# Optimization experiments

Hardware: AMD Instinct MI355X
Metric: run time of the kernel (lower is better)

The kernel has to match this reference:

```python
import jax, jax.numpy as jnp
import numpy as np

B, C, H, W, L, R = 1, 32, 96, 128, 2, 3
N = 2 * R + 1
EPS = 1e-5


def conv2d(x, w, stride=1, pad=1):
    return jax.lax.conv_general_dilated(
        x, w, (stride, stride), ((pad, pad), (pad, pad)),
        dimension_numbers=('NCHW', 'OIHW', 'NCHW'))


def conv_transpose2d(x, w, stride=2, pad=1):
    # torch ConvTranspose2d semantics; w: [Cin, Cout, kH, kW]
    kh, kw = w.shape[2], w.shape[3]
    wf = jnp.flip(w, (2, 3)).transpose(1, 0, 2, 3)  # [Cout, Cin, kh, kw]
    return jax.lax.conv_general_dilated(
        x, wf, (1, 1),
        ((kh - 1 - pad, kh - 1 - pad), (kw - 1 - pad, kw - 1 - pad)),
        lhs_dilation=(stride, stride),
        dimension_numbers=('NCHW', 'OIHW', 'NCHW'))


def bnorm(x, s, b, m, v):
    # inference-mode BatchNorm2d (fixed running stats)
    inv = s * jax.lax.rsqrt(v + EPS)
    return x * inv[None, :, None, None] + (b - m * inv)[None, :, None, None]


def grid_sample(img, grid):
    # bilinear, align_corners=True, padding_mode='zeros'
    # img [B,C,H,W], grid [B,Hg,Wg,2] (x,y) in [-1,1]
    Bi, Ci, Hi, Wi = img.shape
    gx = (grid[..., 0] + 1.0) * 0.5 * (Wi - 1)
    gy = (grid[..., 1] + 1.0) * 0.5 * (Hi - 1)
    x0 = jnp.floor(gx)
    y0 = jnp.floor(gy)
    wx = (gx - x0)[:, None]  # [B,1,Hg,Wg]
    wy = (gy - y0)[:, None]

    def tap(yf, xf):
        valid = (xf >= 0) & (xf <= Wi - 1) & (yf >= 0) & (yf <= Hi - 1)
        xc = jnp.clip(xf, 0, Wi - 1).astype(jnp.int32)
        yc = jnp.clip(yf, 0, Hi - 1).astype(jnp.int32)
        v = jax.vmap(lambda im, y, x: im[:, y, x])(img, yc, xc)  # [B,C,Hg,Wg]
        return v * valid[:, None].astype(img.dtype)

    v00 = tap(y0, x0)
    v01 = tap(y0, x0 + 1)
    v10 = tap(y0 + 1, x0)
    v11 = tap(y0 + 1, x0 + 1)
    return (v00 * (1 - wx) * (1 - wy) + v01 * wx * (1 - wy)
            + v10 * (1 - wx) * wy + v11 * wx * wy)


def _forward(fmap1_0, fmap1_1, fmap2_0, fmap2_1, coords,
             cw1, cw2, cw3, cw4, ctw5, cw6, cb6,
             bn1s, bn1b, bn1m, bn1v, bn2s, bn2b, bn2m, bn2v,
             bn3s, bn3b, bn3m, bn3v, bn4s, bn4b, bn4m, bn4v,
             bn5s, bn5b, bn5m, bn5v, dap_w):
    n = N
    dx = jnp.linspace(-R, R, n)
    delta = jnp.stack(jnp.meshgrid(dx, dx, indexing='ij'), axis=-1)  # [n,n,2]
    b, _, h, w = coords.shape
    cp = coords.transpose(0, 2, 3, 1)  # [b,h,w,2] (x,y)
    bns = ((bn1s, bn1b, bn1m, bn1v), (bn2s, bn2b, bn2m, bn2v),
           (bn3s, bn3b, bn3m, bn3v), (bn4s, bn4b, bn4m, bn4v),
           (bn5s, bn5b, bn5m, bn5v))
    out = []
    for i, (f1, f2) in enumerate(((fmap1_0, fmap2_0), (fmap1_1, fmap2_1))):
        c, h2, w2 = f1.shape[1], f1.shape[2], f1.shape[3]
        # [b,n,h,n,w,2]: first n axis pairs with h, second with w (as in torch view)
        cent = cp[:, None, :, None, :, :] / (2.0 ** i) + delta[None, :, None, :, None, :]
        gx = 2.0 * cent[..., 0] / (w2 - 1) - 1.0
        gy = 2.0 * cent[..., 1] / (h2 - 1) - 1.0
        grid = jnp.stack([gx, gy], -1).reshape(b, n * h, n * w, 2)
        f2s = grid_sample(f2, grid).reshape(b, c, n, h, n, w)
        f2s = f2s.transpose(0, 2, 4, 1, 3, 5)  # [b,du,dv,c,h,w]
        f1e = jnp.broadcast_to(f1[:, None, None], (b, n, n, c, h, w))
        x = jnp.concatenate([f1e, f2s], axis=3).reshape(b * n * n, 2 * c, h, w)
        # MatchingNet (DICL): conv-bn-relu stack, stride-2 down + transposed up
        x = jax.nn.relu(bnorm(conv2d(x, cw1[i]), *(p[i] for p in bns[0])))
        x = jax.nn.relu(bnorm(conv2d(x, cw2[i], stride=2), *(p[i] for p in bns[1])))
        x = jax.nn.relu(bnorm(conv2d(x, cw3[i]), *(p[i] for p in bns[2])))
        x = jax.nn.relu(bnorm(conv2d(x, cw4[i]), *(p[i] for p in bns[3])))
        x = jax.nn.relu(bnorm(conv_transpose2d(x, ctw5[i]), *(p[i] for p in bns[4])))
        x = conv2d(x, cw6[i]) + cb6[i][None, :, None, None]  # [b*n*n,1,h,w]
        cost = x.reshape(b, n * n, h, w)
        # DisplacementAwareProjection: 1x1 conv over the 49 displacement channels
        cost = jnp.einsum('pq,bqhw->bphw', dap_w[i], cost)
        out.append(cost)
    return jnp.concatenate(out, axis=1)  # [b, L*(2r+1)^2, h, w]


def setup_inputs():
    key = jax.random.key(0)
    ks = jax.random.split(key, 40)

    def rn(k, shape, scale=1.0):
        return jax.random.normal(k, shape, jnp.float32) * scale

    inp = {}
    inp['fmap1_0'] = rn(ks[0], (B, C, H, W))
    inp['fmap2_0'] = rn(ks[1], (B, C, H, W))
    inp['fmap1_1'] = rn(ks[2], (B, C, H, W))
    inp['fmap2_1'] = rn(ks[3], (B, C, H, W))
    gy, gx = jnp.meshgrid(jnp.arange(H, dtype=jnp.float32),
                          jnp.arange(W, dtype=jnp.float32), indexing='ij')
    base = jnp.stack([gx, gy], 0)[None]  # [1,2,H,W] (x,y) pixel coords
    inp['coords'] = base + rn(ks[4], (B, 2, H, W), 2.0)

    def cw(k, co, ci, kk):
        return rn(k, (L, co, ci, kk, kk), 1.0 / np.sqrt(ci * kk * kk))

    inp['cw1'] = cw(ks[5], 96, 2 * C, 3)
    inp['cw2'] = cw(ks[6], 128, 96, 3)
    inp['cw3'] = cw(ks[7], 128, 128, 3)
    inp['cw4'] = cw(ks[8], 64, 128, 3)
    inp['ctw5'] = rn(ks[9], (L, 64, 32, 4, 4), 1.0 / np.sqrt(64 * 16))
    inp['cw6'] = cw(ks[10], 1, 32, 3)
    inp['cb6'] = rn(ks[11], (L, 1), 0.1)
    for j, ch in enumerate((96, 128, 128, 64, 32), start=1):
        k4 = jax.random.split(ks[11 + j], 4)
        inp['bn%ds' % j] = 1.0 + rn(k4[0], (L, ch), 0.1)
        inp['bn%db' % j] = rn(k4[1], (L, ch), 0.1)
        inp['bn%dm' % j] = rn(k4[2], (L, ch), 0.1)
        inp['bn%dv' % j] = 1.0 + rn(k4[3], (L, ch), 0.1) ** 2
    # DAP identity init
    inp['dap_w'] = jnp.tile(jnp.eye(N * N, dtype=jnp.float32)[None], (L, 1, 1))
    return inp


def reference(fmap1_0, fmap1_1, fmap2_0, fmap2_1, coords,
              cw1, cw2, cw3, cw4, ctw5, cw6, cb6,
              bn1s, bn1b, bn1m, bn1v, bn2s, bn2b, bn2m, bn2v,
              bn3s, bn3b, bn3m, bn3v, bn4s, bn4b, bn4m, bn4v,
              bn5s, bn5b, bn5m, bn5v, dap_w):
    return _forward(fmap1_0, fmap1_1, fmap2_0, fmap2_1, coords,
                    cw1, cw2, cw3, cw4, ctw5, cw6, cb6,
                    bn1s, bn1b, bn1m, bn1v, bn2s, bn2b, bn2m, bn2v,
                    bn3s, bn3b, bn3m, bn3v, bn4s, bn4b, bn4m, bn4v,
                    bn5s, bn5b, bn5m, bn5v, dap_w)
```

## Files before the change

### kernel.cpp

```cpp
#include <hip/hip_runtime.h>

#define EPSF 1e-5f

typedef __attribute__((ext_vector_type(8))) short short8;
typedef __attribute__((ext_vector_type(4))) float f32x4;

__device__ __forceinline__ ushort f2bf(float x) {
    union { float f; unsigned u; } c; c.f = x;
    unsigned r = c.u + 0x7FFF + ((c.u >> 16) & 1);
    return (ushort)(r >> 16);
}
__device__ __forceinline__ float bf2f(ushort b) {
    union { unsigned u; float f; } c; c.u = ((unsigned)b) << 16;
    return c.f;
}
__device__ __forceinline__ int swz(int a) {
    return a ^ (((a >> 7) & 7) << 4);
}


__global__ __launch_bounds__(256) void k_repack_conv(
    const float* __restrict__ src, ushort* __restrict__ dst, int CO, int CI)
{
    int idx = blockIdx.x * 256 + threadIdx.x;
    if (idx >= CO * CI * 9) return;
    int co = idx / (CI * 9);
    int rem = idx % (CI * 9);
    int ci = rem / 9, tap = rem % 9;
    dst[((size_t)tap * CO + co) * CI + ci] = f2bf(src[idx]);
}

__global__ __launch_bounds__(256) void k_repack_ct(
    const float* __restrict__ src, ushort* __restrict__ dst)
{
    int idx = blockIdx.x * 256 + threadIdx.x;
    if (idx >= 4 * 4 * 32 * 64) return;
    int ci = idx & 63;
    int t = idx >> 6;
    int co = t & 31; t >>= 5;
    int tap = t & 3;
    int parity = t >> 2;
    int ph = parity >> 1, pw = parity & 1;
    int a = tap >> 1, b = tap & 1;
    int kh = ((ph + 1) & 1) + 2 * a;
    int kw = ((pw + 1) & 1) + 2 * b;
    dst[idx] = f2bf(src[((ci * 32 + co) * 4 + kh) * 4 + kw]);
}

__global__ __launch_bounds__(256) void k_sample_nhwc(
    const float* __restrict__ f1_0, const float* __restrict__ f1_1,
    const float* __restrict__ f2_0, const float* __restrict__ f2_1,
    const float* __restrict__ coords, ushort* __restrict__ x0, int d0)
{
    const int HW = 12288;
    const int sp = blockIdx.x * 256 + threadIdx.x;
    const int slot = blockIdx.z;
    const int p = d0 + slot;
    const int l = p / 49;
    const int d = p - l * 49;
    const int du = d / 7, dv = d % 7;
    const float inv_scale = l ? 0.5f : 1.0f;
    const float* f1 = l ? f1_1 : f1_0;
    const float* f2 = l ? f2_1 : f2_0;

    float cx = coords[sp] * inv_scale + (float)(du - 3);
    float cy = coords[HW + sp] * inv_scale + (float)(dv - 3);
    float xf = floorf(cx), yf = floorf(cy);
    float wx = cx - xf, wy = cy - yf;
    int xi = (int)xf, yi = (int)yf;
    float vx0 = (xf >= 0.f && xf <= 127.f) ? 1.f : 0.f;
    float vx1 = (xf + 1.f >= 0.f && xf + 1.f <= 127.f) ? 1.f : 0.f;
    float vy0 = (yf >= 0.f && yf <= 95.f) ? 1.f : 0.f;
    float vy1 = (yf + 1.f >= 0.f && yf + 1.f <= 95.f) ? 1.f : 0.f;
    int x0i = min(max(xi, 0), 127), x1i = min(max(xi + 1, 0), 127);
    int y0i = min(max(yi, 0), 95),  y1i = min(max(yi + 1, 0), 95);
    float w00 = (1.f - wx) * (1.f - wy) * vx0 * vy0;
    float w01 = wx * (1.f - wy) * vx1 * vy0;
    float w10 = (1.f - wx) * wy * vx0 * vy1;
    float w11 = wx * wy * vx1 * vy1;
    int o00 = y0i * 128 + x0i, o01 = y0i * 128 + x1i;
    int o10 = y1i * 128 + x0i, o11 = y1i * 128 + x1i;

    ushort* dst = x0 + ((size_t)slot * HW + sp) * 64;
    #pragma unroll
    for (int g = 0; g < 4; ++g) {
        uint4 pk;
        uint* pw_ = (uint*)&pk;
        #pragma unroll
        for (int q = 0; q < 4; ++q) {
            int c = g * 8 + q * 2;
            pw_[q] = (uint)f2bf(f1[(size_t)c * HW + sp])
                   | ((uint)f2bf(f1[(size_t)(c + 1) * HW + sp]) << 16);
        }
        *(uint4*)(dst + g * 8) = pk;
    }
    #pragma unroll
    for (int g = 0; g < 4; ++g) {
        uint4 pk;
        uint* pw_ = (uint*)&pk;
        #pragma unroll
        for (int q = 0; q < 4; ++q) {
            uint wv = 0;
            #pragma unroll
            for (int h = 0; h < 2; ++h) {
                int c = g * 8 + q * 2 + h;
                const float* fc = f2 + (size_t)c * HW;
                float s = w00 * fc[o00] + w01 * fc[o01] + w10 * fc[o10] + w11 * fc[o11];
                wv |= ((uint)f2bf(s)) << (16 * h);
            }
            pw_[q] = wv;
        }
        *(uint4*)(dst + 32 + g * 8) = pk;
    }
}

template <int CIN, int COUT, int ROWS, int IH, int IW>
__global__ __launch_bounds__(512) void k_conv_lds8(
    const ushort* __restrict__ in, ushort* __restrict__ out,
    const ushort* __restrict__ wbase, int wlstride,
    const float* __restrict__ bs0, const float* __restrict__ bb0,
    const float* __restrict__ bm0, const float* __restrict__ bv0, int d0)
{
    constexpr int NFT = ROWS / 16;
    constexpr int CC = CIN / 64;
    constexpr int NCT = IW / 64;
    constexpr int AB = 10 * 66 * 128;
    constexpr int PB = 3 * ROWS * 128;
    constexpr int SA = (AB + 8191) / 8192;
    constexpr int SB = (PB + 8191) / 8192;
    constexpr int NPH = 3 * CC;
    __shared__ __align__(16) char smem[AB + 2 * PB];
    char* As = smem;

    const int tid = threadIdx.x;
    const int lane = tid & 63, wid = tid >> 6;
    const int lr = lane & 15, kg = lane >> 4;
    const int rt = (int)blockIdx.x / NCT, ct = (int)blockIdx.x % NCT;
    const int r0 = rt * 8, c0 = ct * 64;
    const int co0 = blockIdx.y * ROWS;
    const int slot = blockIdx.z;
    const int l = (d0 + slot) / 49;

    int aoff[SA]; unsigned awr = 0, avalid = 0;
    #pragma unroll
    for (int i = 0; i < SA; ++i) {
        int lin = i * 8192 + tid * 16;
        bool wr = lin < AB;
        int linc = wr ? lin : 0;
        int pos = linc >> 7;
        int prow = (pos * 994) >> 16;
        int pcol = pos - prow * 66;
        int grow = r0 - 1 + prow, gcol = c0 - 1 + pcol;
        bool ok = wr && ((unsigned)grow < (unsigned)IH) && ((unsigned)gcol < (unsigned)IW);
        if (wr) awr |= 1u << i;
        if (ok) avalid |= 1u << i;
        int growc = min(max(grow, 0), IH - 1), gcolc = min(max(gcol, 0), IW - 1);
        aoff[i] = (growc * IW + gcolc) * CIN + ((linc & 127) >> 1);
    }
    int boff[SB]; unsigned bmask = 0;
    #pragma unroll
    for (int i = 0; i < SB; ++i) {
        int lin = i * 8192 + tid * 16;
        if (lin < PB) bmask |= 1u << i;
        int lc = min(lin, PB - 16);
        int rowidx = lc >> 7;
        int tpg = rowidx / ROWS, r = rowidx - tpg * ROWS;
        boff[i] = (tpg * COUT + co0 + r) * CIN + ((lc & 127) >> 1);
    }

    const ushort* ib = in + (size_t)slot * IH * IW * CIN;
    const ushort* wl = wbase + (size_t)l * wlstride;
    const short8 z8 = {0, 0, 0, 0, 0, 0, 0, 0};

    short8 stgA[SA], stgB[SB];
    auto loadA = [&](int cc) {
        #pragma unroll
        for (int i = 0; i < SA; ++i) {
            if ((avalid >> i) & 1) stgA[i] = *(const short8*)(ib + aoff[i] + cc * 64);
            else stgA[i] = z8;
        }
    };
    auto writeA = [&]() {
        #pragma unroll
        for (int i = 0; i < SA; ++i) {
            int lin = i * 8192 + tid * 16;
            if ((awr >> i) & 1)
                *(short8*)(As + swz(lin)) = stgA[i];
        }
    };
    auto loadB = [&](int ps) {
        int pg = ps % 3, cc = ps / 3;
        const ushort* src = wl + pg * (3 * COUT * CIN) + cc * 64;
        #pragma unroll
        for (int i = 0; i < SB; ++i)
            if ((bmask >> i) & 1) stgB[i] = *(const short8*)(src + boff[i]);
    };
    auto writeB = [&](int ps) {
        char* Bs = smem + AB + (ps & 1) * PB;
        #pragma unroll
        for (int i = 0; i < SB; ++i) {
            int lin = i * 8192 + tid * 16;
            if ((bmask >> i) & 1)
                *(short8*)(Bs + swz(lin)) = stgB[i];
        }
    };

    f32x4 acc[4][NFT];
    #pragma unroll
    for (int mf = 0; mf < 4; ++mf)
        #pragma unroll
        for (int nf = 0; nf < NFT; ++nf)
            acc[mf][nf] = (f32x4){0.f, 0.f, 0.f, 0.f};

    loadA(0); loadB(0);
    writeA(); writeB(0);
    __syncthreads();

    #pragma unroll 1
    for (int ps = 0; ps < NPH; ++ps) {
        const int pg = ps % 3;
        const bool hasNext = (ps + 1 < NPH);
        const bool newA = (CC > 1) && (pg == 2) && hasNext;
        if (hasNext) loadB(ps + 1);
        if (newA) loadA(ps / 3 + 1);

        const char* Bs = smem + AB + (ps & 1) * PB;
        #pragma unroll
        for (int kw = 0; kw < 3; ++kw) {
            const int spb = (wid + pg) * 66 + lr + kw;
            #pragma unroll
            for (int ks = 0; ks < 2; ++ks) {
                short8 a[4];
                #pragma unroll
                for (int mf = 0; mf < 4; ++mf) {
                    int sp = spb + mf * 16;
                    a[mf] = *(const short8*)(As + swz(sp * 128 + ks * 64 + kg * 16));
                }
                #pragma unroll
                for (int nf = 0; nf < NFT; ++nf) {
                    int rb = kw * ROWS + nf * 16 + lr;
                    short8 b = *(const short8*)(Bs + swz(rb * 128 + ks * 64 + kg * 16));
                    #pragma unroll
                    for (int mf = 0; mf < 4; ++mf)
                        acc[mf][nf] = __builtin_amdgcn_mfma_f32_16x16x32_bf16(
                            a[mf], b, acc[mf][nf], 0, 0, 0);
                }
            }
        }

        __syncthreads();
        if (hasNext) writeB(ps + 1);
        if (newA) writeA();
        if (hasNext) __syncthreads();
    }

    const float* bs = bs0 + l * COUT;
    const float* bb = bb0 + l * COUT;
    const float* bm = bm0 + l * COUT;
    const float* bv = bv0 + l * COUT;
    ushort* ob = out + (size_t)slot * IH * IW * COUT;
    const int orow = r0 + wid;
    #pragma unroll
    for (int nf = 0; nf < NFT; ++nf) {
        const int col = co0 + nf * 16 + lr;
        const float inv = bs[col] * rsqrtf(bv[col] + EPSF);
        const float beta = bb[col] - bm[col] * inv;
        #pragma unroll
        for (int mf = 0; mf < 4; ++mf) {
            #pragma unroll
            for (int j = 0; j < 4; ++j) {
                int ocol = c0 + mf * 16 + kg * 4 + j;
                float y = fmaxf(fmaf(acc[mf][nf][j], inv, beta), 0.f);
                ob[((size_t)orow * IW + ocol) * COUT + col] = f2bf(y);
            }
        }
    }
}

__global__ __launch_bounds__(512) void k_conv_s2_8(
    const ushort* __restrict__ in, ushort* __restrict__ out,
    const ushort* __restrict__ wbase, int wlstride,
    const float* __restrict__ bs0, const float* __restrict__ bb0,
    const float* __restrict__ bm0, const float* __restrict__ bv0, int d0)
{
    constexpr int AB = 9 * 130 * 64;
    constexpr int PB = 3 * 128 * 64;
    constexpr int SA = (AB + 8191) / 8192;
    constexpr int SB = PB / 8192;
    constexpr int NPH = 9;
    __shared__ __align__(16) char smem[AB + 2 * PB];
    char* As = smem;

    const int tid = threadIdx.x;
    const int lane = tid & 63, wid = tid >> 6;
    const int lr = lane & 15, kg = lane >> 4;
    const int mw = wid >> 1, ch = wid & 1;
    const int r0 = (int)blockIdx.x * 4;
    const int slot = blockIdx.z;
    const int l = (d0 + slot) / 49;

    int aoff[SA]; unsigned awr = 0, avalid = 0;
    #pragma unroll
    for (int i = 0; i < SA; ++i) {
        int lin = i * 8192 + tid * 16;
        bool wr = lin < AB;
        int linc = wr ? lin : 0;
        int pos = linc >> 6;
        int prow = (pos * 2017) >> 18;
        int pcol = pos - prow * 130;
        int grow = 2 * r0 - 1 + prow, gcol = pcol - 1;
        bool ok = wr && ((unsigned)grow < 96u) && ((unsigned)gcol < 128u);
        if (wr) awr |= 1u << i;
        if (ok) avalid |= 1u << i;
        int growc = min(max(grow, 0), 95), gcolc = min(max(gcol, 0), 127);
        aoff[i] = (growc * 128 + gcolc) * 96 + ((linc & 63) >> 1);
    }
    int boff[SB];
    #pragma unroll
    for (int i = 0; i < SB; ++i) {
        int lin = i * 8192 + tid * 16;
        int rowidx = lin >> 6;
        int tpg = rowidx >> 7, r = rowidx & 127;
        boff[i] = ((tpg * 128 + r) * 96) + ((lin & 63) >> 1);
    }

    const ushort* ib = in + (size_t)slot * 12288 * 96;
    const ushort* wl = wbase + (size_t)l * wlstride;
    const short8 z8 = {0, 0, 0, 0, 0, 0, 0, 0};

    short8 stgA[SA], stgB[SB];
    auto loadA = [&](int cc) {
        #pragma unroll
        for (int i = 0; i < SA; ++i) {
            if ((avalid >> i) & 1) stgA[i] = *(const short8*)(ib + aoff[i] + cc * 32);
            else stgA[i] = z8;
        }
    };
    auto writeA = [&]() {
        #pragma unroll
        for (int i = 0; i < SA; ++i) {
            int lin = i * 8192 + tid * 16;
            if ((awr >> i) & 1)
                *(short8*)(As + swz(lin)) = stgA[i];
        }
    };
    auto loadB = [&](int ps) {
        int pg = ps % 3, cc = ps / 3;
        const ushort* src = wl + pg * (3 * 128 * 96) + cc * 32;
        #pragma unroll
        for (int i = 0; i < SB; ++i)
            stgB[i] = *(const short8*)(src + boff[i]);
    };
    auto writeB = [&](int ps) {
        char* Bs = smem + AB + (ps & 1) * PB;
        #pragma unroll
        for (int i = 0; i < SB; ++i) {
            int lin = i * 8192 + tid * 16;
            *(short8*)(Bs + swz(lin)) = stgB[i];
        }
    };

    f32x4 acc[4][4];
    #pragma unroll
    for (int mf = 0; mf < 4; ++mf)
        #pragma unroll
        for (int nf = 0; nf < 4; ++nf)
            acc[mf][nf] = (f32x4){0.f, 0.f, 0.f, 0.f};

    loadA(0); loadB(0);
    writeA(); writeB(0);
    __syncthreads();

    #pragma unroll 1
    for (int ps = 0; ps < NPH; ++ps) {
        const int pg = ps % 3;
        const bool hasNext = (ps + 1 < NPH);
        const bool newA = (pg == 2) && hasNext;
        if (hasNext) loadB(ps + 1);
        if (newA) loadA(ps / 3 + 1);

        const char* Bs = smem + AB + (ps & 1) * PB;
        #pragma unroll
        for (int kw = 0; kw < 3; ++kw) {
            short8 a[4];
            #pragma unroll
            for (int mf = 0; mf < 4; ++mf) {
                int pos = (2 * mw + pg) * 130 + 2 * (mf * 16 + lr) + kw;
                a[mf] = *(const short8*)(As + swz(pos * 64 + kg * 16));
            }
            #pragma unroll
            for (int nf = 0; nf < 4; ++nf) {
                int rb = kw * 128 + ch * 64 + nf * 16 + lr;
                short8 b = *(const short8*)(Bs + swz(rb * 64 + kg * 16));
                #pragma unroll
                for (int mf = 0; mf < 4; ++mf)
                    acc[mf][nf] = __builtin_amdgcn_mfma_f32_16x16x32_bf16(
                        a[mf], b, acc[mf][nf], 0, 0, 0);
            }
        }

        __syncthreads();
        if (hasNext) writeB(ps + 1);
        if (newA) writeA();
        if (hasNext) __syncthreads();
    }

    const float* bs = bs0 + l * 128;
    const float* bb = bb0 + l * 128;
    const float* bm = bm0 + l * 128;
    const float* bv = bv0 + l * 128;
    ushort* ob = out + (size_t)slot * 3072 * 128;
    const int orow = r0 + mw;
    #pragma unroll
    for (int nf = 0; nf < 4; ++nf) {
        const int col = ch * 64 + nf * 16 + lr;
        const float inv = bs[col] * rsqrtf(bv[col] + EPSF);
        const float beta = bb[col] - bm[col] * inv;
        #pragma unroll
        for (int mf = 0; mf < 4; ++mf) {
            #pragma unroll
            for (int j = 0; j < 4; ++j) {
                int ocol = mf * 16 + kg * 4 + j;
                float y = fmaxf(fmaf(acc[mf][nf][j], inv, beta), 0.f);
                ob[((size_t)orow * 64 + ocol) * 128 + col] = f2bf(y);
            }
        }
    }
}

__global__ __launch_bounds__(256) void k_convt_mfma(
    const ushort* __restrict__ in, ushort* __restrict__ out,
    const ushort* __restrict__ wbase,
    const float* __restrict__ bs0, const float* __restrict__ bb0,
    const float* __restrict__ bm0, const float* __restrict__ bv0, int d0)
{
    constexpr int SLICE = 4 * 32 * 128;
    constexpr int S = 4;
    __shared__ __align__(16) char smem[SLICE];

    const int tid = threadIdx.x;
    const int lane = tid & 63, wid = tid >> 6;
    const int lr = lane & 15, kg = lane >> 4;
    const int m0 = blockIdx.x * 256 + wid * 64;
    const int parity = blockIdx.y;
    const int slot = blockIdx.z;
    const int l = (d0 + slot) / 49;
    const int ph = parity >> 1, pw = parity & 1;
    const int kh0 = (ph + 1) & 1, kw0 = (pw + 1) & 1;

    {
        const char* wsrc = (const char*)(wbase + (size_t)l * (16 * 32 * 64));
        #pragma unroll
        for (int i = 0; i < S; ++i) {
            int lin = i * 4096 + tid * 16;
            int rowidx = lin >> 7;
            int tap = rowidx >> 5, r = rowidx & 31;
            short8 v = *(const short8*)(wsrc
                + (((size_t)(parity * 4 + tap) * 32 + r) * 64) * 2 + (lin & 127));
            *(short8*)(smem + swz(lin)) = v;
        }
    }
    __syncthreads();

    int ihA[4], iwA[4];
    #pragma unroll
    for (int mf = 0; mf < 4; ++mf) {
        int m = m0 + mf * 16 + lr;
        int q = m >> 6, r = m & 63;
        ihA[mf] = (2 * q + ph + 1 - kh0) >> 1;
        iwA[mf] = (2 * r + pw + 1 - kw0) >> 1;
    }
    const ushort* ib = in + (size_t)slot * 3072 * 64;

    const short8 z8 = {0, 0, 0, 0, 0, 0, 0, 0};
    f32x4 acc[4][2];
    #pragma unroll
    for (int mf = 0; mf < 4; ++mf)
        #pragma unroll
        for (int nf = 0; nf < 2; ++nf)
            acc[mf][nf] = (f32x4){0.f, 0.f, 0.f, 0.f};

    #pragma unroll
    for (int a = 0; a < 2; ++a) {
        #pragma unroll
        for (int b2 = 0; b2 < 2; ++b2) {
            int srcoff[4]; bool val[4];
            #pragma unroll
            for (int mf = 0; mf < 4; ++mf) {
                int ih = ihA[mf] - a;
                int iw = iwA[mf] - b2;
                val[mf] = ((unsigned)ih < 48u) && ((unsigned)iw < 64u);
                int ihc = min(max(ih, 0), 47), iwc = min(max(iw, 0), 63);
                srcoff[mf] = (ihc * 64 + iwc) * 64;
            }
            const int tap = a * 2 + b2;
            #pragma unroll
            for (int cc = 0; cc < 2; ++cc) {
                const int kbase = cc * 32 + kg * 8;
                short8 av[4];
                #pragma unroll
                for (int mf = 0; mf < 4; ++mf) {
                    short8 v = *(const short8*)(ib + srcoff[mf] + kbase);
                    av[mf] = val[mf] ? v : z8;
                }
                #pragma unroll
                for (int nf = 0; nf < 2; ++nf) {
                    short8 bfr = *(const short8*)(smem
                        + swz((tap * 32 + nf * 16 + lr) * 128 + cc * 64 + kg * 16));
                    #pragma unroll
                    for (int mf = 0; mf < 4; ++mf)
                        acc[mf][nf] = __builtin_amdgcn_mfma_f32_16x16x32_bf16(
                            av[mf], bfr, acc[mf][nf], 0, 0, 0);
                }
            }
        }
    }

    const float* bs = bs0 + l * 32;
    const float* bb = bb0 + l * 32;
    const float* bm = bm0 + l * 32;
    const float* bv = bv0 + l * 32;
    ushort* ob = out + (size_t)slot * 12288 * 32;
    #pragma unroll
    for (int nf = 0; nf < 2; ++nf) {
        const int col = nf * 16 + lr;
        const float inv = bs[col] * rsqrtf(bv[col] + EPSF);
        const float beta = bb[col] - bm[col] * inv;
        #pragma unroll
        for (int mf = 0; mf < 4; ++mf) {
            #pragma unroll
            for (int j = 0; j < 4; ++j) {
                int m = m0 + mf * 16 + kg * 4 + j;
                int q = m >> 6, r = m & 63;
                int sp = (2 * q + ph) * 128 + (2 * r + pw);
                float y = fmaxf(fmaf(acc[mf][nf][j], inv, beta), 0.f);
                ob[(size_t)sp * 32 + col] = f2bf(y);
            }
        }
    }
}

__global__ __launch_bounds__(256) void k_conv6(
    const ushort* __restrict__ x5, float* __restrict__ cost,
    const float* __restrict__ w0, const float* __restrict__ cb6, int d0)
{
    const int sp = blockIdx.x * 256 + threadIdx.x;
    const int slot = blockIdx.z;
    const int p = d0 + slot;
    const int l = p / 49;
    const float* w = w0 + l * 288;
    const int oh = sp >> 7, ow = sp & 127;
    float acc = 0.f;
    #pragma unroll
    for (int kh = 0; kh < 3; ++kh) {
        const int ih = oh - 1 + kh;
        if (ih < 0 || ih >= 96) continue;
        #pragma unroll
        for (int kw = 0; kw < 3; ++kw) {
            const int iw = ow - 1 + kw;
            if (iw < 0 || iw >= 128) continue;
            const ushort* q = x5 + ((size_t)slot * 12288 + ih * 128 + iw) * 32;
            const int tap = kh * 3 + kw;
            #pragma unroll
            for (int g = 0; g < 4; ++g) {
                uint4 v = *(const uint4*)(q + g * 8);
                const uint* vw = (const uint*)&v;
                #pragma unroll
                for (int t = 0; t < 4; ++t) {
                    int ci = g * 8 + t * 2;
                    acc = fmaf(bf2f((ushort)(vw[t] & 0xFFFF)), w[ci * 9 + tap], acc);
                    acc = fmaf(bf2f((ushort)(vw[t] >> 16)), w[(ci + 1) * 9 + tap], acc);
                }
            }
        }
    }
    cost[(size_t)p * 12288 + sp] = acc + cb6[l];
}

__global__ __launch_bounds__(256) void k_dap(
    const float* __restrict__ cost, const float* __restrict__ dw,
    float* __restrict__ out)
{
    const int sp = blockIdx.x * 256 + threadIdx.x;
    const int p = blockIdx.y;
    const float* dr = dw + p * 49;
    float acc = 0.f;
    #pragma unroll
    for (int q = 0; q < 49; ++q)
        acc = fmaf(dr[q], cost[(size_t)q * 12288 + sp], acc);
    out[(size_t)p * 12288 + sp] = acc;
}

extern "C" void kernel_launch(void* const* d_in, const int* in_sizes, int n_in,
                              void* d_out, int out_size, void* d_ws, size_t ws_size,
                              hipStream_t stream)
{
    const float* fm1_0 = (const float*)d_in[0];
    const float* fm2_0 = (const float*)d_in[1];
    const float* fm1_1 = (const float*)d_in[2];
    const float* fm2_1 = (const float*)d_in[3];
    const float* coords = (const float*)d_in[4];
    const float* cw1  = (const float*)d_in[5];
    const float* cw2  = (const float*)d_in[6];
    const float* cw3  = (const float*)d_in[7];
    const float* cw4  = (const float*)d_in[8];
    const float* ctw5 = (const float*)d_in[9];
    const float* cw6  = (const float*)d_in[10];
    const float* cb6  = (const float*)d_in[11];
    const float* bn[5][4];
    for (int j = 0; j < 5; ++j)
        for (int k = 0; k < 4; ++k)
            bn[j][k] = (const float*)d_in[12 + j * 4 + k];
    const float* dap = (const float*)d_in[32];
    float* out = (float*)d_out;

    const size_t A_US = 786432;
    const size_t B_US = 1179648;
    const size_t W1 = 9 * 96 * 64, W2 = 9 * 128 * 96, W3 = 9 * 128 * 128;
    const size_t W4 = 9 * 64 * 128, W5 = 16 * 32 * 64;
    const size_t W_US = 2 * (W1 + W2 + W3 + W4 + W5);
    const size_t COSTF = (size_t)98 * 12288;

    int DC = 1;
    for (int cand : {98, 66, 49, 42, 33, 25, 17, 13, 9, 7, 5, 3, 2, 1}) {
        size_t need = (A_US + B_US) * (size_t)cand * 2 + W_US * 2 + COSTF * 4 + 4096;
        if (need <= ws_size) { DC = cand; break; }
    }

    ushort* bufA = (ushort*)d_ws;
    ushort* bufB = bufA + A_US * DC;
    ushort* wp = bufB + B_US * DC;
    ushort* wr1 = wp; wp += 2 * W1;
    ushort* wr2 = wp; wp += 2 * W2;
    ushort* wr3 = wp; wp += 2 * W3;
    ushort* wr4 = wp; wp += 2 * W4;
    ushort* wr5 = wp; wp += 2 * W5;
    float* cost = (float*)wp;

    for (int l = 0; l < 2; ++l) {
        k_repack_conv<<<dim3(216), 256, 0, stream>>>(cw1 + (size_t)l * W1, wr1 + l * W1, 96, 64);
        k_repack_conv<<<dim3(432), 256, 0, stream>>>(cw2 + (size_t)l * W2, wr2 + l * W2, 128, 96);
        k_repack_conv<<<dim3(576), 256, 0, stream>>>(cw3 + (size_t)l * W3, wr3 + l * W3, 128, 128);
        k_repack_conv<<<dim3(288), 256, 0, stream>>>(cw4 + (size_t)l * W4, wr4 + l * W4, 64, 128);
        k_repack_ct<<<dim3(128), 256, 0, stream>>>(ctw5 + (size_t)l * W5, wr5 + l * W5);
    }

    for (int d0 = 0; d0 < 98; d0 += DC) {
        const int ndd = min(DC, 98 - d0);
        k_sample_nhwc<<<dim3(48, 1, ndd), 256, 0, stream>>>(
            fm1_0, fm1_1, fm2_0, fm2_1, coords, bufA, d0);
        k_conv_lds8<64, 96, 96, 96, 128>
            <<<dim3(24, 1, ndd), 512, 0, stream>>>(bufA, bufB, wr1, (int)W1,
                bn[0][0], bn[0][1], bn[0][2], bn[0][3], d0);
        k_conv_s2_8<<<dim3(12, 1, ndd), 512, 0, stream>>>(bufB, bufA, wr2, (int)W2,
                bn[1][0], bn[1][1], bn[1][2], bn[1][3], d0);
        k_conv_lds8<128, 128, 64, 48, 64>
            <<<dim3(6, 2, ndd), 512, 0, stream>>>(bufA, bufB, wr3, (int)W3,
                bn[2][0], bn[2][1], bn[2][2], bn[2][3], d0);
        k_conv_lds8<128, 64, 64, 48, 64>
            <<<dim3(6, 1, ndd), 512, 0, stream>>>(bufB, bufA, wr4, (int)W4,
                bn[3][0], bn[3][1], bn[3][2], bn[3][3], d0);
        k_convt_mfma<<<dim3(12, 4, ndd), 256, 0, stream>>>(bufA, bufB, wr5,
                bn[4][0], bn[4][1], bn[4][2], bn[4][3], d0);
        k_conv6<<<dim3(48, 1, ndd), 256, 0, stream>>>(
            bufB, cost, cw6, cb6, d0);
    }
    for (int l = 0; l < 2; ++l)
        k_dap<<<dim3(48, 49), 256, 0, stream>>>(
            cost + (size_t)l * 49 * 12288, dap + (size_t)l * 49 * 49,
            out + (size_t)l * 49 * 12288);
}
```

Baseline: 826.8 us.

## Precompute displacement-invariant fmap1 half of first conv once per level

The first conv's input concatenates fmap1 (identical for all 49 displacements) with sampled fmap2. The fmap1 half's partial conv result is now computed once per level into an fp32 buffer, and each displacement only convolves the 32 sampled channels, starting from that precomputed partial sum. This roughly halves the first conv's MACs and the sampler's writes. In exchange, each block must read a large fp32 accumulator preload, and a new specialized conv kernel with its own epilogue is introduced.

```diff
diff --git a/kernel.cpp b/kernel.cpp
--- a/kernel.cpp
+++ b/kernel.cpp
@@ -47,10 +47,28 @@
     dst[idx] = f2bf(src[((ci * 32 + co) * 4 + kh) * 4 + kw]);
 }
 
+__global__ __launch_bounds__(256) void k_pack_f1(
+    const float* __restrict__ f1, ushort* __restrict__ xf1)
+{
+    const int sp = blockIdx.x * 256 + threadIdx.x;
+    ushort* dst = xf1 + (size_t)sp * 32;
+    #pragma unroll
+    for (int g = 0; g < 4; ++g) {
+        uint4 pk;
+        uint* pw_ = (uint*)&pk;
+        #pragma unroll
+        for (int q = 0; q < 4; ++q) {
+            int c = g * 8 + q * 2;
+            pw_[q] = (uint)f2bf(f1[(size_t)c * 12288 + sp])
+                   | ((uint)f2bf(f1[(size_t)(c + 1) * 12288 + sp]) << 16);
+        }
+        *(uint4*)(dst + g * 8) = pk;
+    }
+}
+
 __global__ __launch_bounds__(256) void k_sample_nhwc(
-    const float* __restrict__ f1_0, const float* __restrict__ f1_1,
     const float* __restrict__ f2_0, const float* __restrict__ f2_1,
-    const float* __restrict__ coords, ushort* __restrict__ x0, int d0)
+    const float* __restrict__ coords, ushort* __restrict__ x0s, int d0)
 {
     const int HW = 12288;
     const int sp = blockIdx.x * 256 + threadIdx.x;
@@ -60,7 +78,6 @@
     const int d = p - l * 49;
     const int du = d / 7, dv = d % 7;
     const float inv_scale = l ? 0.5f : 1.0f;
-    const float* f1 = l ? f1_1 : f1_0;
     const float* f2 = l ? f2_1 : f2_0;
 
     float cx = coords[sp] * inv_scale + (float)(du - 3);
@@ -81,19 +98,7 @@
     int o00 = y0i * 128 + x0i, o01 = y0i * 128 + x1i;
     int o10 = y1i * 128 + x0i, o11 = y1i * 128 + x1i;
 
-    ushort* dst = x0 + ((size_t)slot * HW + sp) * 64;
-    #pragma unroll
-    for (int g = 0; g < 4; ++g) {
-        uint4 pk;
-        uint* pw_ = (uint*)&pk;
-        #pragma unroll
-        for (int q = 0; q < 4; ++q) {
-            int c = g * 8 + q * 2;
-            pw_[q] = (uint)f2bf(f1[(size_t)c * HW + sp])
-                   | ((uint)f2bf(f1[(size_t)(c + 1) * HW + sp]) << 16);
-        }
-        *(uint4*)(dst + g * 8) = pk;
-    }
+    ushort* dst = x0s + ((size_t)slot * HW + sp) * 32;
     #pragma unroll
     for (int g = 0; g < 4; ++g) {
         uint4 pk;
@@ -110,7 +115,154 @@
             }
             pw_[q] = wv;
         }
-        *(uint4*)(dst + 32 + g * 8) = pk;
+        *(uint4*)(dst + g * 8) = pk;
+    }
+}
+
+template <int EPI>
+__global__ __launch_bounds__(512) void k_conv1(
+    const ushort* __restrict__ in,
+    ushort* __restrict__ out,
+    const ushort* __restrict__ wbase,
+    const float* __restrict__ p1,
+    const float* __restrict__ bs0, const float* __restrict__ bb0,
+    const float* __restrict__ bm0, const float* __restrict__ bv0,
+    int d0, int koff)
+{
+    constexpr int AB = 10 * 130 * 64;
+    constexpr int PB = 3 * 96 * 64;
+    __shared__ __align__(16) char smem[AB + 2 * PB];
+    char* As = smem;
+
+    const int tid = threadIdx.x;
+    const int lane = tid & 63, wid = tid >> 6;
+    const int lr = lane & 15, kg = lane >> 4;
+    const int rt = blockIdx.x;
+    const int r0 = rt * 8;
+    const int slot = blockIdx.z;
+    const int l = (d0 + slot) / 49;
+
+    const ushort* ib = in + (size_t)slot * 12288 * 32;
+    const ushort* wl = wbase + (size_t)l * (9 * 96 * 64);
+    const short8 z8 = {0, 0, 0, 0, 0, 0, 0, 0};
+
+    #pragma unroll
+    for (int i = 0; i < 11; ++i) {
+        int lin = i * 8192 + tid * 16;
+        if (lin < AB) {
+            int pos = lin >> 6;
+            int prow = (pos * 2017) >> 18;
+            int pcol = pos - prow * 130;
+            int grow = r0 - 1 + prow, gcol = pcol - 1;
+            bool ok = ((unsigned)grow < 96u) && ((unsigned)gcol < 128u);
+            short8 v = z8;
+            if (ok) v = *(const short8*)(ib + (grow * 128 + gcol) * 32 + ((lin & 63) >> 1));
+            *(short8*)(As + swz(lin)) = v;
+        }
+    }
+
+    int boff[3]; unsigned bmask = 0;
+    #pragma unroll
+    for (int i = 0; i < 3; ++i) {
+        int lin = i * 8192 + tid * 16;
+        if (lin < PB) bmask |= 1u << i;
+        int lc = min(lin, PB - 16);
+        int rowidx = lc >> 6;
+        int tpg = (rowidx * 683) >> 16;
+        int r = rowidx - tpg * 96;
+        boff[i] = (tpg * 96 + r) * 64 + koff + ((lc & 63) >> 1);
+    }
+    short8 stgB[3];
+    auto loadB = [&](int pg) {
+        const ushort* src = wl + pg * (3 * 96 * 64);
+        #pragma unroll
+        for (int i = 0; i < 3; ++i)
+            if ((bmask >> i) & 1) stgB[i] = *(const short8*)(src + boff[i]);
+    };
+    auto writeB = [&](int pg) {
+        char* Bs = smem + AB + (pg & 1) * PB;
+        #pragma unroll
+        for (int i = 0; i < 3; ++i) {
+            int lin = i * 8192 + tid * 16;
+            if ((bmask >> i) & 1) *(short8*)(Bs + swz(lin)) = stgB[i];
+        }
+    };
+
+    f32x4 acc[8][6];
+    if constexpr (EPI == 0) {
+        const float* pl = p1 + (size_t)l * 1179648
+                        + ((size_t)(rt * 512 + tid)) * 192;
+        #pragma unroll
+        for (int mf = 0; mf < 8; ++mf)
+            #pragma unroll
+            for (int nf = 0; nf < 6; ++nf)
+                acc[mf][nf] = *(const f32x4*)(pl + (mf * 6 + nf) * 4);
+    } else {
+        #pragma unroll
+        for (int mf = 0; mf < 8; ++mf)
+            #pragma unroll
+            for (int nf = 0; nf < 6; ++nf)
+                acc[mf][nf] = (f32x4){0.f, 0.f, 0.f, 0.f};
+    }
+
+    loadB(0);
+    writeB(0);
+    __syncthreads();
+
+    #pragma unroll
+    for (int ps = 0; ps < 3; ++ps) {
+        if (ps < 2) loadB(ps + 1);
+        const char* Bs = smem + AB + (ps & 1) * PB;
+        #pragma unroll
+        for (int kw = 0; kw < 3; ++kw) {
+            short8 a[8];
+            #pragma unroll
+            for (int mf = 0; mf < 8; ++mf) {
+                int sp = (wid + ps) * 130 + mf * 16 + lr + kw;
+                a[mf] = *(const short8*)(As + swz(sp * 64 + kg * 16));
+            }
+            #pragma unroll
+            for (int nf = 0; nf < 6; ++nf) {
+                short8 b = *(const short8*)(Bs + swz((kw * 96 + nf * 16 + lr) * 64 + kg * 16));
+                #pragma unroll
+                for (int mf = 0; mf < 8; ++mf)
+                    acc[mf][nf] = __builtin_amdgcn_mfma_f32_16x16x32_bf16(
+                        a[mf], b, acc[mf][nf], 0, 0, 0);
+            }
+        }
+        __syncthreads();
+        if (ps < 2) { writeB(ps + 1); __syncthreads(); }
+    }
+
+    if constexpr (EPI == 1) {
+        float* of = (float*)out + ((size_t)(rt * 512 + tid)) * 192;
+        #pragma unroll
+        for (int mf = 0; mf < 8; ++mf)
+            #pragma unroll
+            for (int nf = 0; nf < 6; ++nf)
+                *(f32x4*)(of + (mf * 6 + nf) * 4) = acc[mf][nf];
+    } else {
+        const float* bs = bs0 + l * 96;
+        const float* bb = bb0 + l * 96;
+        const float* bm = bm0 + l * 96;
+        const float* bv = bv0 + l * 96;
+        ushort* ob = out + (size_t)slot * 12288 * 96;
+        const int orow = r0 + wid;
+        #pragma unroll
+        for (int nf = 0; nf < 6; ++nf) {
+            const int col = nf * 16 + lr;
+            const float inv = bs[col] * rsqrtf(bv[col] + EPSF);
+            const float beta = bb[col] - bm[col] * inv;
+            #pragma unroll
+            for (int mf = 0; mf < 8; ++mf) {
+                #pragma unroll
+                for (int j = 0; j < 4; ++j) {
+                    int ocol = mf * 16 + kg * 4 + j;
+                    float y = fmaxf(fmaf(acc[mf][nf][j], inv, beta), 0.f);
+                    ob[((size_t)orow * 128 + ocol) * 96 + col] = f2bf(y);
+                }
+            }
+        }
     }
 }
 
@@ -614,28 +766,33 @@
     const float* dap = (const float*)d_in[32];
     float* out = (float*)d_out;
 
-    const size_t A_US = 786432;
+    const size_t A_US = 393216;
     const size_t B_US = 1179648;
+    const size_t XF1 = 393216;
     const size_t W1 = 9 * 96 * 64, W2 = 9 * 128 * 96, W3 = 9 * 128 * 128;
     const size_t W4 = 9 * 64 * 128, W5 = 16 * 32 * 64;
     const size_t W_US = 2 * (W1 + W2 + W3 + W4 + W5);
+    const size_t P1F = 2 * (size_t)12 * 512 * 192;
     const size_t COSTF = (size_t)98 * 12288;
 
     int DC = 1;
     for (int cand : {98, 66, 49, 42, 33, 25, 17, 13, 9, 7, 5, 3, 2, 1}) {
-        size_t need = (A_US + B_US) * (size_t)cand * 2 + W_US * 2 + COSTF * 4 + 4096;
+        size_t need = (A_US + B_US) * (size_t)cand * 2 + (XF1 + W_US) * 2
+                    + (P1F + COSTF) * 4 + 4096;
         if (need <= ws_size) { DC = cand; break; }
     }
 
     ushort* bufA = (ushort*)d_ws;
     ushort* bufB = bufA + A_US * DC;
-    ushort* wp = bufB + B_US * DC;
+    ushort* xf1 = bufB + B_US * DC;
+    ushort* wp = xf1 + XF1;
     ushort* wr1 = wp; wp += 2 * W1;
     ushort* wr2 = wp; wp += 2 * W2;
     ushort* wr3 = wp; wp += 2 * W3;
     ushort* wr4 = wp; wp += 2 * W4;
     ushort* wr5 = wp; wp += 2 * W5;
-    float* cost = (float*)wp;
+    float* P1 = (float*)wp;
+    float* cost = P1 + P1F;
 
     for (int l = 0; l < 2; ++l) {
         k_repack_conv<<<dim3(216), 256, 0, stream>>>(cw1 + (size_t)l * W1, wr1 + l * W1, 96, 64);
@@ -645,13 +802,20 @@
         k_repack_ct<<<dim3(128), 256, 0, stream>>>(ctw5 + (size_t)l * W5, wr5 + l * W5);
     }
 
+    for (int l = 0; l < 2; ++l) {
+        k_pack_f1<<<dim3(48), 256, 0, stream>>>(l ? fm1_1 : fm1_0, xf1);
+        k_conv1<1><<<dim3(12, 1, 1), 512, 0, stream>>>(
+            xf1, (ushort*)(P1 + (size_t)l * 1179648), wr1, nullptr,
+            bn[0][0], bn[0][1], bn[0][2], bn[0][3], l * 49, 0);
+    }
+
     for (int d0 = 0; d0 < 98; d0 += DC) {
         const int ndd = min(DC, 98 - d0);
         k_sample_nhwc<<<dim3(48, 1, ndd), 256, 0, stream>>>(
-            fm1_0, fm1_1, fm2_0, fm2_1, coords, bufA, d0);
-        k_conv_lds8<64, 96, 96, 96, 128>
-            <<<dim3(24, 1, ndd), 512, 0, stream>>>(bufA, bufB, wr1, (int)W1,
-                bn[0][0], bn[0][1], bn[0][2], bn[0][3], d0);
+            fm2_0, fm2_1, coords, bufA, d0);
+        k_conv1<0><<<dim3(12, 1, ndd), 512, 0, stream>>>(
+            bufA, bufB, wr1, P1,
+            bn[0][0], bn[0][1], bn[0][2], bn[0][3], d0, 32);
         k_conv_s2_8<<<dim3(12, 1, ndd), 512, 0, stream>>>(bufB, bufA, wr2, (int)W2,
                 bn[1][0], bn[1][1], bn[1][2], bn[1][3], d0);
         k_conv_lds8<128, 128, 64, 48, 64>
```

Measured after the change: 1.147 ms. 38.8% more time.
